# Kernel optimization log

Measured on AMD Instinct MI355X. Metric: run time of the kernel, lower is better.

## Reference

```python
import jax, jax.numpy as jnp
import numpy as np

EPS = 1e-6  # torch nn.PairwiseDistance default eps


def setup_inputs() -> dict:
    key = jax.random.key(0)
    k1, k2 = jax.random.split(key)
    B, D, H, W = 4096, 512, 128, 128
    x = jax.random.normal(k1, (B, D), dtype=jnp.float32)
    weight = jax.random.normal(k2, (D, H * W), dtype=jnp.float32)  # SOM codebook (D, K)
    xs, ys = jnp.meshgrid(jnp.arange(H), jnp.arange(W), indexing="ij")
    locations = jnp.stack([xs.ravel(), ys.ravel()], axis=-1).astype(jnp.float32)  # (K, 2)
    return {"x": x, "weight": weight, "locations": locations}


def reference(x, weight, locations):
    # Faithful to torch: dists[b,k] = ||x[b,:] - weight[:,k] + eps||_2 reduced over D,
    # then min over codes, gather BMU grid locations, mean min-distance loss.
    B, D = x.shape
    x2 = jnp.sum(x * x, axis=1, keepdims=True)            # (B,1)
    w2 = jnp.sum(weight * weight, axis=0, keepdims=True)  # (1,K)
    cross = x @ weight                                     # (B,K) GEMM
    # exact expansion of sum_d (x - w + eps)^2
    lin = 2.0 * EPS * (jnp.sum(x, axis=1, keepdims=True) - jnp.sum(weight, axis=0, keepdims=True))
    d2 = x2 - 2.0 * cross + w2 + lin + jnp.float32(D) * EPS * EPS  # (B,K)
    dists = jnp.sqrt(jnp.maximum(d2, 0.0))
    losses = jnp.min(dists, axis=1, keepdims=True)         # (B,1)
    bmu_idx = jnp.argmin(dists, axis=1)                    # (B,)
    bmu_locations = locations[bmu_idx][:, None, :]         # (B,1,2) like locations[bmu_indexes]
    loss = jnp.sum(losses) / jnp.float32(B)
    return bmu_locations, loss
```

## Files before the change

### kernel.cpp

```cpp
#include <hip/hip_runtime.h>
#include <stdint.h>

#define B_ROWS 4096
#define D_DIM  512
#define K_CODES 16384
#define EPS 1e-6f

typedef __attribute__((ext_vector_type(8))) short short8;
typedef __attribute__((ext_vector_type(4))) float floatx4;

__device__ __forceinline__ unsigned short f2bf(float f) {
  unsigned int u = __float_as_uint(f);
  u += 0x7FFFu + ((u >> 16) & 1u);
  return (unsigned short)(u >> 16);
}
__device__ __forceinline__ float bf2f(unsigned short h) {
  return __uint_as_float(((unsigned int)h) << 16);
}

__device__ __forceinline__ void load_lds16(const short* g, short* l) {
  __builtin_amdgcn_global_load_lds(
      (const __attribute__((address_space(1))) void*)g,
      (__attribute__((address_space(3))) void*)l, 16, 0, 0);
}

__global__ void prep_x_kernel(const float* __restrict__ x,
                              short* __restrict__ A,
                              float* __restrict__ row_term,
                              float* __restrict__ loss_acc,
                              unsigned int* __restrict__ counter) {
  const int b = blockIdx.x;
  const int t = threadIdx.x;
  if (b == 0 && t == 0) { loss_acc[0] = 0.0f; counter[0] = 0u; }
  const float* xr = x + (size_t)b * D_DIM;
  float4 v0 = ((const float4*)xr)[t * 2];
  float4 v1 = ((const float4*)xr)[t * 2 + 1];
  float vals[8] = {v0.x, v0.y, v0.z, v0.w, v1.x, v1.y, v1.z, v1.w};
  short8 hi, lo;
  float s = 0.f, q = 0.f;
#pragma unroll
  for (int i = 0; i < 8; ++i) {
    float v = vals[i];
    s += v;
    q += v * v;
    unsigned short h = f2bf(v);
    float r = v - bf2f(h);
    hi[i] = (short)h;
    lo[i] = (short)f2bf(r);
  }
  *(short8*)(A + (size_t)b * 1024 + t * 8) = hi;
  *(short8*)(A + (size_t)b * 1024 + 512 + t * 8) = lo;
#pragma unroll
  for (int m = 1; m < 64; m <<= 1) {
    s += __shfl_xor(s, m, 64);
    q += __shfl_xor(q, m, 64);
  }
  if (t == 0) row_term[b] = q + 2.0f * EPS * s + (float)D_DIM * EPS * EPS;
}

__global__ void prep_w_kernel(const float* __restrict__ w,
                              short* __restrict__ W,
                              float* __restrict__ col_term) {
  __shared__ float tile[64][65];
  __shared__ float red[2][64][4];
  const int k0 = blockIdx.x * 64;
  const int t = threadIdx.x;
  const int kl = t & 63;
  const int dg = t >> 6;
  float s = 0.f, q = 0.f;
  for (int d0 = 0; d0 < D_DIM; d0 += 64) {
    __syncthreads();
#pragma unroll
    for (int i = 0; i < 16; ++i) {
      int idx = i * 256 + t;
      int r = idx >> 6, c = idx & 63;
      tile[r][c] = w[(size_t)(d0 + r) * K_CODES + k0 + c];
    }
    __syncthreads();
#pragma unroll
    for (int j = 0; j < 16; ++j) {
      float v = tile[dg * 16 + j][kl];
      s += v;
      q += v * v;
    }
#pragma unroll
    for (int i = 0; i < 16; ++i) {
      int idx = i * 256 + t;
      int rk = idx >> 6, cd = idx & 63;
      float v = tile[cd][rk];
      unsigned short h = f2bf(v);
      float r2 = v - bf2f(h);
      W[(size_t)(k0 + rk) * 1024 + d0 + cd] = (short)h;
      W[(size_t)(k0 + rk) * 1024 + 512 + d0 + cd] = (short)f2bf(r2);
    }
  }
  red[0][kl][dg] = s;
  red[1][kl][dg] = q;
  __syncthreads();
  if (t < 64) {
    float ss = red[0][t][0] + red[0][t][1] + red[0][t][2] + red[0][t][3];
    float qq = red[1][t][0] + red[1][t][1] + red[1][t][2] + red[1][t][3];
    col_term[k0 + t] = qq - 2.0f * EPS * ss;
  }
}

__global__ __launch_bounds__(256, 3) void som_gemm_kernel(
    const short* __restrict__ A, const short* __restrict__ W,
    const float* __restrict__ row_term, const float* __restrict__ col_term,
    unsigned long long* __restrict__ partial) {
  __shared__ __align__(16) short As[128 * 64];
  __shared__ __align__(16) short Bs[128 * 64];

  const int nt = blockIdx.x;
  const int mt = blockIdx.y;
  const int m0 = mt * 128, n0 = nt * 128;
  const int tid = threadIdx.x;
  const int wv = tid >> 6, lane = tid & 63;
  const int m_off = (wv & 1) * 64, n_off = (wv >> 1) * 64;
  const int q = lane >> 4, l15 = lane & 15;

  floatx4 acc[4][4];
  const floatx4 zero = {0.f, 0.f, 0.f, 0.f};
#pragma unroll
  for (int mi = 0; mi < 4; ++mi)
#pragma unroll
    for (int ni = 0; ni < 4; ++ni) acc[mi][ni] = zero;

  const int srow = lane >> 3;
  const int scol = ((lane & 7) ^ (srow & 7)) * 8;

  for (int kt = 0; kt < 24; ++kt) {
    const int a_k0 = (kt * 64) & 1023;
    const int w_k0 = (kt < 16) ? ((kt * 64) & 511) : (kt * 64 - 512);
    __syncthreads();
#pragma unroll
    for (int i = 0; i < 4; ++i) {
      const int c = wv * 4 + i;
      const int row = c * 8 + srow;
      load_lds16(A + (size_t)(m0 + row) * 1024 + a_k0 + scol, As + c * 512);
      load_lds16(W + (size_t)(n0 + row) * 1024 + w_k0 + scol, Bs + c * 512);
    }
    __syncthreads();
#pragma unroll
    for (int ks = 0; ks < 2; ++ks) {
      short8 af[4], bf[4];
#pragma unroll
      for (int mi = 0; mi < 4; ++mi)
        af[mi] = *(const short8*)(As + (m_off + mi * 16 + l15) * 64 +
                                  (((ks * 4 + q) ^ (l15 & 7)) * 8));
#pragma unroll
      for (int ni = 0; ni < 4; ++ni)
        bf[ni] = *(const short8*)(Bs + (n_off + ni * 16 + l15) * 64 +
                                  (((ks * 4 + q) ^ (l15 & 7)) * 8));
#pragma unroll
      for (int mi = 0; mi < 4; ++mi)
#pragma unroll
        for (int ni = 0; ni < 4; ++ni)
          acc[mi][ni] = __builtin_amdgcn_mfma_f32_16x16x32_bf16(
              af[mi], bf[ni], acc[mi][ni], 0, 0, 0);
    }
  }

  float ct[4];
#pragma unroll
  for (int ni = 0; ni < 4; ++ni) ct[ni] = col_term[n0 + n_off + ni * 16 + l15];
  float rt[16];
#pragma unroll
  for (int mi = 0; mi < 4; ++mi)
#pragma unroll
    for (int r = 0; r < 4; ++r)
      rt[mi * 4 + r] = row_term[m0 + m_off + mi * 16 + q * 4 + r];

  __syncthreads();
  unsigned long long* lds_min = (unsigned long long*)As;

#pragma unroll
  for (int mi = 0; mi < 4; ++mi) {
#pragma unroll
    for (int r = 0; r < 4; ++r) {
      unsigned long long v = ~0ull;
#pragma unroll
      for (int ni = 0; ni < 4; ++ni) {
        float d2 = rt[mi * 4 + r] + ct[ni] - 2.0f * acc[mi][ni][r];
        d2 = fmaxf(d2, 0.0f);
        unsigned long long p =
            ((unsigned long long)__float_as_uint(d2) << 32) |
            (unsigned int)(n0 + n_off + ni * 16 + l15);
        v = p < v ? p : v;
      }
#pragma unroll
      for (int mms = 1; mms < 16; mms <<= 1) {
        unsigned long long o = __shfl_xor(v, mms, 64);
        v = o < v ? o : v;
      }
      if (l15 == 0) lds_min[(wv >> 1) * 128 + m_off + mi * 16 + q * 4 + r] = v;
    }
  }
  __syncthreads();
  if (tid < 128) {
    unsigned long long v0 = lds_min[tid];
    unsigned long long v1 = lds_min[128 + tid];
    partial[(size_t)nt * B_ROWS + m0 + tid] = v1 < v0 ? v1 : v0;
  }
}

__global__ void finalize_kernel(const unsigned long long* __restrict__ partial,
                                const float* __restrict__ loc,
                                float* __restrict__ out,
                                float* __restrict__ loss_acc,
                                unsigned int* __restrict__ counter) {
  __shared__ unsigned long long red[4][64];
  const int t = threadIdx.x;
  const int rl = t & 63;
  const int p = t >> 6;
  const int b = blockIdx.x * 64 + rl;
  unsigned long long v = ~0ull;
#pragma unroll
  for (int i = 0; i < 32; ++i) {
    int nt = p * 32 + i;
    unsigned long long pv = partial[(size_t)nt * B_ROWS + b];
    v = pv < v ? pv : v;
  }
  red[p][rl] = v;
  __syncthreads();
  if (t < 64) {
    unsigned long long v0 = red[0][t], v1 = red[1][t];
    unsigned long long v2 = red[2][t], v3 = red[3][t];
    v0 = v1 < v0 ? v1 : v0;
    v2 = v3 < v2 ? v3 : v2;
    v0 = v2 < v0 ? v2 : v0;
    unsigned int k = (unsigned int)(v0 & 0xFFFFFFFFu);
    float d2 = __uint_as_float((unsigned int)(v0 >> 32));
    float dist = sqrtf(d2);
    int row = blockIdx.x * 64 + t;
    out[2 * row] = loc[2 * k];
    out[2 * row + 1] = loc[2 * k + 1];
    float s = dist;
#pragma unroll
    for (int m = 1; m < 64; m <<= 1) s += __shfl_xor(s, m, 64);
    if (t == 0) {
      atomicAdd(loss_acc, s);
      __threadfence();
      unsigned int old = atomicAdd(counter, 1u);
      if (old == gridDim.x - 1) {
        __threadfence();
        float total = atomicAdd(loss_acc, 0.0f);
        out[2 * B_ROWS] = total * (1.0f / (float)B_ROWS);
      }
    }
  }
}

extern "C" void kernel_launch(void* const* d_in, const int* in_sizes, int n_in,
                              void* d_out, int out_size, void* d_ws, size_t ws_size,
                              hipStream_t stream) {
  const float* x = (const float*)d_in[0];
  const float* w = (const float*)d_in[1];
  const float* loc = (const float*)d_in[2];
  float* out = (float*)d_out;
  char* ws = (char*)d_ws;

  short* A = (short*)(ws + 0);
  short* W = (short*)(ws + 8388608);
  float* row_term = (float*)(ws + 41943040);
  float* col_term = (float*)(ws + 41959424);
  unsigned long long* partial = (unsigned long long*)(ws + 42024960);
  float* loss_acc = (float*)(ws + 46219264);
  unsigned int* counter = (unsigned int*)(ws + 46219268);

  prep_x_kernel<<<B_ROWS, 64, 0, stream>>>(x, A, row_term, loss_acc, counter);
  prep_w_kernel<<<K_CODES / 64, 256, 0, stream>>>(w, W, col_term);
  som_gemm_kernel<<<dim3(K_CODES / 128, B_ROWS / 128), 256, 0, stream>>>(
      A, W, row_term, col_term, partial);
  finalize_kernel<<<B_ROWS / 64, 256, 0, stream>>>(partial, loc, out, loss_acc,
                                                   counter);
}
```

Before: 303.6 us.

## Enlarge GEMM M-tile to 256 and parallelize codebook prep over D

The GEMM tile grows from 128x128 to 256x128 per block, with each wave computing 128x64 using 8x4 MFMA accumulators. This raises arithmetic intensity per LDS load and halves the reads of W, but costs more registers (launch bounds drop to 2 blocks per SIMD) and gives a smaller grid. Codebook preparation is also split across D chunks with vectorized float4 loads and short8 stores. A new reduction kernel then sums the per-chunk column statistics, which are staged in the partial buffer region before that buffer is used.

```diff
diff --git a/kernel.cpp b/kernel.cpp
--- a/kernel.cpp
+++ b/kernel.cpp
@@ -60,69 +60,82 @@
 
 __global__ void prep_w_kernel(const float* __restrict__ w,
                               short* __restrict__ W,
-                              float* __restrict__ col_term) {
+                              float2* __restrict__ colpart) {
   __shared__ float tile[64][65];
-  __shared__ float red[2][64][4];
   const int k0 = blockIdx.x * 64;
+  const int d0 = blockIdx.y * 64;
   const int t = threadIdx.x;
-  const int kl = t & 63;
-  const int dg = t >> 6;
-  float s = 0.f, q = 0.f;
-  for (int d0 = 0; d0 < D_DIM; d0 += 64) {
-    __syncthreads();
-#pragma unroll
-    for (int i = 0; i < 16; ++i) {
-      int idx = i * 256 + t;
-      int r = idx >> 6, c = idx & 63;
-      tile[r][c] = w[(size_t)(d0 + r) * K_CODES + k0 + c];
-    }
-    __syncthreads();
-#pragma unroll
-    for (int j = 0; j < 16; ++j) {
-      float v = tile[dg * 16 + j][kl];
+#pragma unroll
+  for (int i = 0; i < 4; ++i) {
+    int idx = i * 256 + t;
+    int r = idx >> 4, c4 = (idx & 15) * 4;
+    float4 v = *(const float4*)&w[(size_t)(d0 + r) * K_CODES + k0 + c4];
+    tile[r][c4 + 0] = v.x;
+    tile[r][c4 + 1] = v.y;
+    tile[r][c4 + 2] = v.z;
+    tile[r][c4 + 3] = v.w;
+  }
+  __syncthreads();
+  const int sub = t & 7;
+  const int cd8 = sub * 8;
+#pragma unroll
+  for (int g = 0; g < 2; ++g) {
+    const int rk = (t >> 3) + g * 32;
+    short8 hi, lo;
+    float s = 0.f, q = 0.f;
+#pragma unroll
+    for (int j = 0; j < 8; ++j) {
+      float v = tile[cd8 + j][rk];
       s += v;
       q += v * v;
-    }
-#pragma unroll
-    for (int i = 0; i < 16; ++i) {
-      int idx = i * 256 + t;
-      int rk = idx >> 6, cd = idx & 63;
-      float v = tile[cd][rk];
       unsigned short h = f2bf(v);
       float r2 = v - bf2f(h);
-      W[(size_t)(k0 + rk) * 1024 + d0 + cd] = (short)h;
-      W[(size_t)(k0 + rk) * 1024 + 512 + d0 + cd] = (short)f2bf(r2);
-    }
-  }
-  red[0][kl][dg] = s;
-  red[1][kl][dg] = q;
-  __syncthreads();
-  if (t < 64) {
-    float ss = red[0][t][0] + red[0][t][1] + red[0][t][2] + red[0][t][3];
-    float qq = red[1][t][0] + red[1][t][1] + red[1][t][2] + red[1][t][3];
-    col_term[k0 + t] = qq - 2.0f * EPS * ss;
-  }
-}
-
-__global__ __launch_bounds__(256, 3) void som_gemm_kernel(
+      hi[j] = (short)h;
+      lo[j] = (short)f2bf(r2);
+    }
+    *(short8*)(W + (size_t)(k0 + rk) * 1024 + d0 + cd8) = hi;
+    *(short8*)(W + (size_t)(k0 + rk) * 1024 + 512 + d0 + cd8) = lo;
+#pragma unroll
+    for (int m = 1; m < 8; m <<= 1) {
+      s += __shfl_xor(s, m, 64);
+      q += __shfl_xor(q, m, 64);
+    }
+    if (sub == 0) colpart[(size_t)blockIdx.y * K_CODES + k0 + rk] = {s, q};
+  }
+}
+
+__global__ void col_reduce_kernel(const float2* __restrict__ colpart,
+                                  float* __restrict__ col_term) {
+  const int k = blockIdx.x * 256 + threadIdx.x;
+  float s = 0.f, q = 0.f;
+#pragma unroll
+  for (int c = 0; c < 8; ++c) {
+    float2 p = colpart[(size_t)c * K_CODES + k];
+    s += p.x;
+    q += p.y;
+  }
+  col_term[k] = q - 2.0f * EPS * s;
+}
+
+__global__ __launch_bounds__(256, 2) void som_gemm_kernel(
     const short* __restrict__ A, const short* __restrict__ W,
     const float* __restrict__ row_term, const float* __restrict__ col_term,
     unsigned long long* __restrict__ partial) {
-  __shared__ __align__(16) short As[128 * 64];
+  __shared__ __align__(16) short As[256 * 64];
   __shared__ __align__(16) short Bs[128 * 64];
 
   const int nt = blockIdx.x;
   const int mt = blockIdx.y;
-  const int m0 = mt * 128, n0 = nt * 128;
+  const int m0 = mt * 256, n0 = nt * 128;
   const int tid = threadIdx.x;
   const int wv = tid >> 6, lane = tid & 63;
-  const int m_off = (wv & 1) * 64, n_off = (wv >> 1) * 64;
+  const int m_off = (wv & 1) * 128, n_off = (wv >> 1) * 64;
   const int q = lane >> 4, l15 = lane & 15;
 
-  floatx4 acc[4][4];
+  floatx4 acc[8][4];
   const floatx4 zero = {0.f, 0.f, 0.f, 0.f};
 #pragma unroll
-  for (int mi = 0; mi < 4; ++mi)
+  for (int mi = 0; mi < 8; ++mi)
 #pragma unroll
     for (int ni = 0; ni < 4; ++ni) acc[mi][ni] = zero;
 
@@ -134,26 +147,30 @@
     const int w_k0 = (kt < 16) ? ((kt * 64) & 511) : (kt * 64 - 512);
     __syncthreads();
 #pragma unroll
+    for (int i = 0; i < 8; ++i) {
+      const int c = wv * 8 + i;
+      load_lds16(A + (size_t)(m0 + c * 8 + srow) * 1024 + a_k0 + scol,
+                 As + c * 512);
+    }
+#pragma unroll
     for (int i = 0; i < 4; ++i) {
       const int c = wv * 4 + i;
-      const int row = c * 8 + srow;
-      load_lds16(A + (size_t)(m0 + row) * 1024 + a_k0 + scol, As + c * 512);
-      load_lds16(W + (size_t)(n0 + row) * 1024 + w_k0 + scol, Bs + c * 512);
+      load_lds16(W + (size_t)(n0 + c * 8 + srow) * 1024 + w_k0 + scol,
+                 Bs + c * 512);
     }
     __syncthreads();
 #pragma unroll
     for (int ks = 0; ks < 2; ++ks) {
-      short8 af[4], bf[4];
-#pragma unroll
-      for (int mi = 0; mi < 4; ++mi)
-        af[mi] = *(const short8*)(As + (m_off + mi * 16 + l15) * 64 +
-                                  (((ks * 4 + q) ^ (l15 & 7)) * 8));
+      const int sw = ((ks * 4 + q) ^ (l15 & 7)) * 8;
+      short8 af[8], bf[4];
+#pragma unroll
+      for (int mi = 0; mi < 8; ++mi)
+        af[mi] = *(const short8*)(As + (m_off + mi * 16 + l15) * 64 + sw);
 #pragma unroll
       for (int ni = 0; ni < 4; ++ni)
-        bf[ni] = *(const short8*)(Bs + (n_off + ni * 16 + l15) * 64 +
-                                  (((ks * 4 + q) ^ (l15 & 7)) * 8));
-#pragma unroll
-      for (int mi = 0; mi < 4; ++mi)
+        bf[ni] = *(const short8*)(Bs + (n_off + ni * 16 + l15) * 64 + sw);
+#pragma unroll
+      for (int mi = 0; mi < 8; ++mi)
 #pragma unroll
         for (int ni = 0; ni < 4; ++ni)
           acc[mi][ni] = __builtin_amdgcn_mfma_f32_16x16x32_bf16(
@@ -164,24 +181,20 @@
   float ct[4];
 #pragma unroll
   for (int ni = 0; ni < 4; ++ni) ct[ni] = col_term[n0 + n_off + ni * 16 + l15];
-  float rt[16];
-#pragma unroll
-  for (int mi = 0; mi < 4; ++mi)
-#pragma unroll
-    for (int r = 0; r < 4; ++r)
-      rt[mi * 4 + r] = row_term[m0 + m_off + mi * 16 + q * 4 + r];
 
   __syncthreads();
   unsigned long long* lds_min = (unsigned long long*)As;
 
 #pragma unroll
-  for (int mi = 0; mi < 4; ++mi) {
+  for (int mi = 0; mi < 8; ++mi) {
 #pragma unroll
     for (int r = 0; r < 4; ++r) {
+      const int row = m_off + mi * 16 + q * 4 + r;
+      float rtv = row_term[m0 + row];
       unsigned long long v = ~0ull;
 #pragma unroll
       for (int ni = 0; ni < 4; ++ni) {
-        float d2 = rt[mi * 4 + r] + ct[ni] - 2.0f * acc[mi][ni][r];
+        float d2 = rtv + ct[ni] - 2.0f * acc[mi][ni][r];
         d2 = fmaxf(d2, 0.0f);
         unsigned long long p =
             ((unsigned long long)__float_as_uint(d2) << 32) |
@@ -193,13 +206,13 @@
         unsigned long long o = __shfl_xor(v, mms, 64);
         v = o < v ? o : v;
       }
-      if (l15 == 0) lds_min[(wv >> 1) * 128 + m_off + mi * 16 + q * 4 + r] = v;
-    }
-  }
-  __syncthreads();
-  if (tid < 128) {
+      if (l15 == 0) lds_min[(wv >> 1) * 256 + row] = v;
+    }
+  }
+  __syncthreads();
+  {
     unsigned long long v0 = lds_min[tid];
-    unsigned long long v1 = lds_min[128 + tid];
+    unsigned long long v1 = lds_min[256 + tid];
     partial[(size_t)nt * B_ROWS + m0 + tid] = v1 < v0 ? v1 : v0;
   }
 }
@@ -265,12 +278,14 @@
   float* row_term = (float*)(ws + 41943040);
   float* col_term = (float*)(ws + 41959424);
   unsigned long long* partial = (unsigned long long*)(ws + 42024960);
+  float2* colpart = (float2*)(ws + 42024960);
   float* loss_acc = (float*)(ws + 46219264);
   unsigned int* counter = (unsigned int*)(ws + 46219268);
 
   prep_x_kernel<<<B_ROWS, 64, 0, stream>>>(x, A, row_term, loss_acc, counter);
-  prep_w_kernel<<<K_CODES / 64, 256, 0, stream>>>(w, W, col_term);
-  som_gemm_kernel<<<dim3(K_CODES / 128, B_ROWS / 128), 256, 0, stream>>>(
+  prep_w_kernel<<<dim3(K_CODES / 64, D_DIM / 64), 256, 0, stream>>>(w, W, colpart);
+  col_reduce_kernel<<<K_CODES / 256, 256, 0, stream>>>(colpart, col_term);
+  som_gemm_kernel<<<dim3(K_CODES / 128, B_ROWS / 256), 256, 0, stream>>>(
       A, W, row_term, col_term, partial);
   finalize_kernel<<<B_ROWS / 64, 256, 0, stream>>>(partial, loc, out, loss_acc,
                                                    counter);
```

Result: faster. 291.0 us (-4.1%).

## Merge prep kernels and split weight prep over D chunks with partial column sums

Applied to the files above, without the earlier changes.

Fuses the x and weight preparation into one launch and splits the weight transpose/bf16-split across 8 D-chunks per 64-code tile, for 2048 weight blocks instead of 256, using float4 loads and short8 stores. Per-chunk column partial sums go to a buffer that the GEMM epilogue reduces. This targets the low parallelism and scalar 2-byte stores of the old weight prep, and saves one launch. It also raises the GEMM launch-bounds occupancy hint from 3 to 4, which may force register spilling, and adds 8 extra loads per column term in the epilogue.

```diff
diff --git a/kernel.cpp b/kernel.cpp
--- a/kernel.cpp
+++ b/kernel.cpp
@@ -24,89 +24,96 @@
       (__attribute__((address_space(3))) void*)l, 16, 0, 0);
 }
 
-__global__ void prep_x_kernel(const float* __restrict__ x,
-                              short* __restrict__ A,
-                              float* __restrict__ row_term,
-                              float* __restrict__ loss_acc,
-                              unsigned int* __restrict__ counter) {
-  const int b = blockIdx.x;
+__global__ void prep_kernel(const float* __restrict__ x,
+                            const float* __restrict__ w,
+                            short* __restrict__ A, short* __restrict__ W,
+                            float* __restrict__ row_term,
+                            float* __restrict__ colpart,
+                            float* __restrict__ loss_acc,
+                            unsigned int* __restrict__ counter) {
+  const int bid = blockIdx.x;
   const int t = threadIdx.x;
-  if (b == 0 && t == 0) { loss_acc[0] = 0.0f; counter[0] = 0u; }
-  const float* xr = x + (size_t)b * D_DIM;
-  float4 v0 = ((const float4*)xr)[t * 2];
-  float4 v1 = ((const float4*)xr)[t * 2 + 1];
-  float vals[8] = {v0.x, v0.y, v0.z, v0.w, v1.x, v1.y, v1.z, v1.w};
-  short8 hi, lo;
-  float s = 0.f, q = 0.f;
-#pragma unroll
-  for (int i = 0; i < 8; ++i) {
-    float v = vals[i];
-    s += v;
-    q += v * v;
-    unsigned short h = f2bf(v);
-    float r = v - bf2f(h);
-    hi[i] = (short)h;
-    lo[i] = (short)f2bf(r);
-  }
-  *(short8*)(A + (size_t)b * 1024 + t * 8) = hi;
-  *(short8*)(A + (size_t)b * 1024 + 512 + t * 8) = lo;
-#pragma unroll
-  for (int m = 1; m < 64; m <<= 1) {
-    s += __shfl_xor(s, m, 64);
-    q += __shfl_xor(q, m, 64);
-  }
-  if (t == 0) row_term[b] = q + 2.0f * EPS * s + (float)D_DIM * EPS * EPS;
-}
-
-__global__ void prep_w_kernel(const float* __restrict__ w,
-                              short* __restrict__ W,
-                              float* __restrict__ col_term) {
-  __shared__ float tile[64][65];
-  __shared__ float red[2][64][4];
-  const int k0 = blockIdx.x * 64;
-  const int t = threadIdx.x;
-  const int kl = t & 63;
-  const int dg = t >> 6;
-  float s = 0.f, q = 0.f;
-  for (int d0 = 0; d0 < D_DIM; d0 += 64) {
+  if (bid < 2048) {
+    __shared__ float tile[64][65];
+    const int k0 = (bid & 255) * 64;
+    const int dchunk = bid >> 8;
+    const int d0 = dchunk * 64;
+#pragma unroll
+    for (int i = 0; i < 4; ++i) {
+      int idx = i * 256 + t;
+      int r = idx >> 4, c4 = (idx & 15) * 4;
+      float4 v = *(const float4*)&w[(size_t)(d0 + r) * K_CODES + k0 + c4];
+      tile[r][c4 + 0] = v.x;
+      tile[r][c4 + 1] = v.y;
+      tile[r][c4 + 2] = v.z;
+      tile[r][c4 + 3] = v.w;
+    }
     __syncthreads();
-#pragma unroll
-    for (int i = 0; i < 16; ++i) {
-      int idx = i * 256 + t;
-      int r = idx >> 6, c = idx & 63;
-      tile[r][c] = w[(size_t)(d0 + r) * K_CODES + k0 + c];
-    }
-    __syncthreads();
-#pragma unroll
-    for (int j = 0; j < 16; ++j) {
-      float v = tile[dg * 16 + j][kl];
-      s += v;
-      q += v * v;
-    }
-#pragma unroll
-    for (int i = 0; i < 16; ++i) {
-      int idx = i * 256 + t;
-      int rk = idx >> 6, cd = idx & 63;
-      float v = tile[cd][rk];
-      unsigned short h = f2bf(v);
-      float r2 = v - bf2f(h);
-      W[(size_t)(k0 + rk) * 1024 + d0 + cd] = (short)h;
-      W[(size_t)(k0 + rk) * 1024 + 512 + d0 + cd] = (short)f2bf(r2);
-    }
-  }
-  red[0][kl][dg] = s;
-  red[1][kl][dg] = q;
-  __syncthreads();
-  if (t < 64) {
-    float ss = red[0][t][0] + red[0][t][1] + red[0][t][2] + red[0][t][3];
-    float qq = red[1][t][0] + red[1][t][1] + red[1][t][2] + red[1][t][3];
-    col_term[k0 + t] = qq - 2.0f * EPS * ss;
-  }
-}
-
-__global__ __launch_bounds__(256, 3) void som_gemm_kernel(
+    const int sub = t & 7;
+    const int cd8 = sub * 8;
+#pragma unroll
+    for (int g = 0; g < 2; ++g) {
+      const int rk = (t >> 3) + g * 32;
+      short8 hi, lo;
+      float s = 0.f, q = 0.f;
+#pragma unroll
+      for (int j = 0; j < 8; ++j) {
+        float v = tile[cd8 + j][rk];
+        s += v;
+        q += v * v;
+        unsigned short h = f2bf(v);
+        float r2 = v - bf2f(h);
+        hi[j] = (short)h;
+        lo[j] = (short)f2bf(r2);
+      }
+      *(short8*)(W + (size_t)(k0 + rk) * 1024 + d0 + cd8) = hi;
+      *(short8*)(W + (size_t)(k0 + rk) * 1024 + 512 + d0 + cd8) = lo;
+#pragma unroll
+      for (int m = 1; m < 8; m <<= 1) {
+        s += __shfl_xor(s, m, 64);
+        q += __shfl_xor(q, m, 64);
+      }
+      if (sub == 0)
+        colpart[(size_t)dchunk * K_CODES + k0 + rk] = q - 2.0f * EPS * s;
+    }
+  } else {
+    const int xb = bid - 2048;
+    if (xb == 0 && t == 0) { loss_acc[0] = 0.0f; counter[0] = 0u; }
+    const int wv = t >> 6, lane = t & 63;
+#pragma unroll
+    for (int i = 0; i < 4; ++i) {
+      const int b = xb * 16 + i * 4 + wv;
+      const float* xr = x + (size_t)b * D_DIM;
+      float4 v0 = ((const float4*)xr)[lane * 2];
+      float4 v1 = ((const float4*)xr)[lane * 2 + 1];
+      float vals[8] = {v0.x, v0.y, v0.z, v0.w, v1.x, v1.y, v1.z, v1.w};
+      short8 hi, lo;
+      float s = 0.f, q = 0.f;
+#pragma unroll
+      for (int j = 0; j < 8; ++j) {
+        float v = vals[j];
+        s += v;
+        q += v * v;
+        unsigned short h = f2bf(v);
+        float r = v - bf2f(h);
+        hi[j] = (short)h;
+        lo[j] = (short)f2bf(r);
+      }
+      *(short8*)(A + (size_t)b * 1024 + lane * 8) = hi;
+      *(short8*)(A + (size_t)b * 1024 + 512 + lane * 8) = lo;
+#pragma unroll
+      for (int m = 1; m < 64; m <<= 1) {
+        s += __shfl_xor(s, m, 64);
+        q += __shfl_xor(q, m, 64);
+      }
+      if (lane == 0) row_term[b] = q + 2.0f * EPS * s + (float)D_DIM * EPS * EPS;
+    }
+  }
+}
+
+__global__ __launch_bounds__(256, 4) void som_gemm_kernel(
     const short* __restrict__ A, const short* __restrict__ W,
-    const float* __restrict__ row_term, const float* __restrict__ col_term,
+    const float* __restrict__ row_term, const float* __restrict__ colpart,
     unsigned long long* __restrict__ partial) {
   __shared__ __align__(16) short As[128 * 64];
   __shared__ __align__(16) short Bs[128 * 64];
@@ -143,15 +150,14 @@
     __syncthreads();
 #pragma unroll
     for (int ks = 0; ks < 2; ++ks) {
+      const int sw = ((ks * 4 + q) ^ (l15 & 7)) * 8;
       short8 af[4], bf[4];
 #pragma unroll
       for (int mi = 0; mi < 4; ++mi)
-        af[mi] = *(const short8*)(As + (m_off + mi * 16 + l15) * 64 +
-                                  (((ks * 4 + q) ^ (l15 & 7)) * 8));
+        af[mi] = *(const short8*)(As + (m_off + mi * 16 + l15) * 64 + sw);
 #pragma unroll
       for (int ni = 0; ni < 4; ++ni)
-        bf[ni] = *(const short8*)(Bs + (n_off + ni * 16 + l15) * 64 +
-                                  (((ks * 4 + q) ^ (l15 & 7)) * 8));
+        bf[ni] = *(const short8*)(Bs + (n_off + ni * 16 + l15) * 64 + sw);
 #pragma unroll
       for (int mi = 0; mi < 4; ++mi)
 #pragma unroll
@@ -163,7 +169,13 @@
 
   float ct[4];
 #pragma unroll
-  for (int ni = 0; ni < 4; ++ni) ct[ni] = col_term[n0 + n_off + ni * 16 + l15];
+  for (int ni = 0; ni < 4; ++ni) {
+    const int k = n0 + n_off + ni * 16 + l15;
+    float s = 0.f;
+#pragma unroll
+    for (int c = 0; c < 8; ++c) s += colpart[(size_t)c * K_CODES + k];
+    ct[ni] = s;
+  }
   float rt[16];
 #pragma unroll
   for (int mi = 0; mi < 4; ++mi)
@@ -263,15 +275,15 @@
   short* A = (short*)(ws + 0);
   short* W = (short*)(ws + 8388608);
   float* row_term = (float*)(ws + 41943040);
-  float* col_term = (float*)(ws + 41959424);
-  unsigned long long* partial = (unsigned long long*)(ws + 42024960);
-  float* loss_acc = (float*)(ws + 46219264);
-  unsigned int* counter = (unsigned int*)(ws + 46219268);
-
-  prep_x_kernel<<<B_ROWS, 64, 0, stream>>>(x, A, row_term, loss_acc, counter);
-  prep_w_kernel<<<K_CODES / 64, 256, 0, stream>>>(w, W, col_term);
+  float* colpart = (float*)(ws + 41959424);
+  unsigned long long* partial = (unsigned long long*)(ws + 42483712);
+  float* loss_acc = (float*)(ws + 46678016);
+  unsigned int* counter = (unsigned int*)(ws + 46678020);
+
+  prep_kernel<<<2304, 256, 0, stream>>>(x, w, A, W, row_term, colpart,
+                                        loss_acc, counter);
   som_gemm_kernel<<<dim3(K_CODES / 128, B_ROWS / 128), 256, 0, stream>>>(
-      A, W, row_term, col_term, partial);
+      A, W, row_term, colpart, partial);
   finalize_kernel<<<B_ROWS / 64, 256, 0, stream>>>(partial, loc, out, loss_acc,
                                                    counter);
 }
```

Result: faster. 288.9 us (-4.8%).
